# Performance work log

Measured on AMD Instinct MI355X. Metric: run time of the kernel, lower is better.

## Reference

```python
import math
import jax, jax.numpy as jnp
import numpy as np

B, S, HID = 2, 1024, 1024
NH, HD = 16, 64
WIN = 4096
CACHE = 3072
EPS = 1e-5


def _clinear(xr, xi, Wr, Wi, br, bi):
    # complex linear: (xr + i xi)(Wr + i Wi)^T + (br + i bi)
    yr = xr @ Wr.T - xi @ Wi.T + br
    yi = xr @ Wi.T + xi @ Wr.T + bi
    return yr, yi


def _forward(hidden_re, hidden_im, K_cache_re, K_cache_im, V_cache_re, V_cache_im,
             gamma, beta_re, beta_im,
             q_Wr, q_Wi, q_br, q_bi, k_Wr, k_Wi, k_br, k_bi,
             v_Wr, v_Wi, v_br, v_bi, o_Wr, o_Wi, o_br, o_bi):
    batch, seq, _ = hidden_re.shape
    # --- complex LayerNorm: center complex mean, normalize by sqrt(E|x-mu|^2) ---
    mur = hidden_re.mean(-1, keepdims=True)
    mui = hidden_im.mean(-1, keepdims=True)
    cr = hidden_re - mur
    ci = hidden_im - mui
    inv = jax.lax.rsqrt((cr * cr + ci * ci).mean(-1, keepdims=True) + EPS)
    nr = cr * inv * gamma + beta_re
    ni = ci * inv * gamma + beta_im
    # --- projections ---
    Qr, Qi = _clinear(nr, ni, q_Wr, q_Wi, q_br, q_bi)
    Kr, Ki = _clinear(nr, ni, k_Wr, k_Wi, k_br, k_bi)
    Vr, Vi = _clinear(nr, ni, v_Wr, v_Wi, v_br, v_bi)
    Qr = Qr.reshape(batch, seq, NH, HD)
    Qi = Qi.reshape(batch, seq, NH, HD)
    Kr = Kr.reshape(batch, seq, NH, HD)
    Ki = Ki.reshape(batch, seq, NH, HD)
    Vr = Vr.reshape(batch, seq, NH, HD)
    Vi = Vi.reshape(batch, seq, NH, HD)
    # --- KV cache concat + window eviction (static shapes) ---
    cache_len = K_cache_re.shape[1]
    Kr = jnp.concatenate([K_cache_re, Kr], axis=1)
    Ki = jnp.concatenate([K_cache_im, Ki], axis=1)
    Vr = jnp.concatenate([V_cache_re, Vr], axis=1)
    Vi = jnp.concatenate([V_cache_im, Vi], axis=1)
    total_kv = Kr.shape[1]
    if total_kv > WIN:
        drop = total_kv - WIN
        Kr, Ki, Vr, Vi = Kr[:, drop:], Ki[:, drop:], Vr[:, drop:], Vi[:, drop:]
        cache_len = max(0, cache_len - drop)
        total_kv = WIN
    # --- Hermitian scores: Re(Q K^H) = Qr.Kr + Qi.Ki ---
    scale = 1.0 / math.sqrt(HD)
    scores = (jnp.einsum('bshd,bthd->bhst', Qr, Kr)
              + jnp.einsum('bshd,bthd->bhst', Qi, Ki)) * scale
    rows = jnp.arange(seq)[:, None]
    cols = jnp.arange(total_kv)[None, :]
    allowed = cols <= rows + cache_len  # causal within current chunk, full cache visible
    scores = jnp.where(allowed, scores, jnp.float32(-1e30))
    weights = jax.nn.softmax(scores, axis=-1)  # [B,NH,S,T]
    outr = jnp.einsum('bhst,bthd->bshd', weights, Vr).reshape(batch, seq, NH * HD)
    outi = jnp.einsum('bhst,bthd->bshd', weights, Vi).reshape(batch, seq, NH * HD)
    dr, di = _clinear(outr, outi, o_Wr, o_Wi, o_br, o_bi)
    out_re = hidden_re + dr
    out_im = hidden_im + di
    new_K_re, new_K_im = Kr[:, -WIN:], Ki[:, -WIN:]
    new_V_re, new_V_im = Vr[:, -WIN:], Vi[:, -WIN:]
    return out_re, out_im, new_K_re, new_K_im, new_V_re, new_V_im


def setup_inputs() -> dict:
    key = jax.random.key(0)
    ks = jax.random.split(key, 16)
    w = 0.02
    d = {
        'hidden_re': jax.random.normal(ks[0], (B, S, HID), jnp.float32),
        'hidden_im': jax.random.normal(ks[1], (B, S, HID), jnp.float32),
        'K_cache_re': jax.random.normal(ks[2], (B, CACHE, NH, HD), jnp.float32),
        'K_cache_im': jax.random.normal(ks[3], (B, CACHE, NH, HD), jnp.float32),
        'V_cache_re': jax.random.normal(ks[4], (B, CACHE, NH, HD), jnp.float32),
        'V_cache_im': jax.random.normal(ks[5], (B, CACHE, NH, HD), jnp.float32),
        'gamma': jnp.ones((HID,), jnp.float32),
        'beta_re': jnp.zeros((HID,), jnp.float32),
        'beta_im': jnp.zeros((HID,), jnp.float32),
    }
    for i, p in enumerate(['q', 'k', 'v', 'o']):
        d[p + '_Wr'] = jax.random.normal(ks[6 + 2 * i], (HID, HID), jnp.float32) * w
        d[p + '_Wi'] = jax.random.normal(ks[7 + 2 * i], (HID, HID), jnp.float32) * w
        d[p + '_br'] = jnp.zeros((HID,), jnp.float32)
        d[p + '_bi'] = jnp.zeros((HID,), jnp.float32)
    return d


def reference(hidden_re, hidden_im, K_cache_re, K_cache_im, V_cache_re, V_cache_im,
              gamma, beta_re, beta_im,
              q_Wr, q_Wi, q_br, q_bi, k_Wr, k_Wi, k_br, k_bi,
              v_Wr, v_Wi, v_br, v_bi, o_Wr, o_Wi, o_br, o_bi):
    return _forward(hidden_re, hidden_im, K_cache_re, K_cache_im, V_cache_re, V_cache_im,
                    gamma, beta_re, beta_im,
                    q_Wr, q_Wi, q_br, q_bi, k_Wr, k_Wi, k_br, k_bi,
                    v_Wr, v_Wi, v_br, v_bi, o_Wr, o_Wi, o_br, o_bi)
```

## Files before the change

### kernel.cpp

```cpp
#include <hip/hip_runtime.h>
#include <hip/hip_bf16.h>
#include <cstdint>
#include <cstddef>

typedef __bf16 bf16x8 __attribute__((ext_vector_type(8)));
typedef float  f32x4  __attribute__((ext_vector_type(4)));

__device__ __forceinline__ unsigned short f2bf(float f) {
  union { float f; unsigned u; } v; v.f = f;
  unsigned u = v.u;
  u += 0x7FFFu + ((u >> 16) & 1u);
  return (unsigned short)(u >> 16);
}

__device__ __forceinline__ unsigned short f2bf_cvt(float f) {
  __bf16 h = (__bf16)f;
  return __builtin_bit_cast(unsigned short, h);
}

struct alignas(16) US8 { unsigned short u[8]; };

__device__ __forceinline__ void g2lds16(const void* g, void* l) {
  __builtin_amdgcn_global_load_lds(
      (const __attribute__((address_space(1))) unsigned int*)g,
      (__attribute__((address_space(3))) unsigned int*)l, 16, 0, 0);
}

#define BB 2
#define SS 1024
#define HID 1024
#define NHH 16
#define HDD 64
#define TT 4096
#define CCH 3072

__global__ __launch_bounds__(256) void ln_kernel(
    const float* __restrict__ hre, const float* __restrict__ him,
    const float* __restrict__ gamma, const float* __restrict__ bre,
    const float* __restrict__ bim, unsigned short* __restrict__ Aln)
{
  int m = blockIdx.x;
  int tid = threadIdx.x;
  const float4 vr = ((const float4*)(hre + (size_t)m * HID))[tid];
  const float4 vi = ((const float4*)(him + (size_t)m * HID))[tid];
  float sr = vr.x + vr.y + vr.z + vr.w;
  float si = vi.x + vi.y + vi.z + vi.w;
  float sq = vr.x*vr.x + vr.y*vr.y + vr.z*vr.z + vr.w*vr.w
           + vi.x*vi.x + vi.y*vi.y + vi.z*vi.z + vi.w*vi.w;
  __shared__ float red[3][4];
  int lane = tid & 63, w = tid >> 6;
  for (int off = 32; off; off >>= 1) {
    sr += __shfl_down(sr, off, 64);
    si += __shfl_down(si, off, 64);
    sq += __shfl_down(sq, off, 64);
  }
  if (lane == 0) { red[0][w] = sr; red[1][w] = si; red[2][w] = sq; }
  __syncthreads();
  sr = red[0][0] + red[0][1] + red[0][2] + red[0][3];
  si = red[1][0] + red[1][1] + red[1][2] + red[1][3];
  sq = red[2][0] + red[2][1] + red[2][2] + red[2][3];
  float mur = sr * (1.f/1024.f), mui = si * (1.f/1024.f);
  float var = sq * (1.f/1024.f) - mur*mur - mui*mui;
  float inv = rsqrtf(var + 1e-5f);
  int k = tid * 4;
  float4 g  = ((const float4*)gamma)[tid];
  float4 br = ((const float4*)bre)[tid];
  float4 bi = ((const float4*)bim)[tid];
  ushort4 nr, ni;
  nr.x = f2bf((vr.x - mur) * inv * g.x + br.x);
  nr.y = f2bf((vr.y - mur) * inv * g.y + br.y);
  nr.z = f2bf((vr.z - mur) * inv * g.z + br.z);
  nr.w = f2bf((vr.w - mur) * inv * g.w + br.w);
  ni.x = f2bf((vi.x - mui) * inv * g.x + bi.x);
  ni.y = f2bf((vi.y - mui) * inv * g.y + bi.y);
  ni.z = f2bf((vi.z - mui) * inv * g.z + bi.z);
  ni.w = f2bf((vi.w - mui) * inv * g.w + bi.w);
  *(ushort4*)&Aln[(size_t)m * 2048 + k]        = nr;
  *(ushort4*)&Aln[(size_t)m * 2048 + 1024 + k] = ni;
}

__global__ __launch_bounds__(256) void wprep_kernel(
    const float* __restrict__ qWr, const float* __restrict__ qWi,
    const float* __restrict__ kWr, const float* __restrict__ kWi,
    const float* __restrict__ vWr, const float* __restrict__ vWi,
    const float* __restrict__ oWr, const float* __restrict__ oWi,
    unsigned short* __restrict__ Wc)
{
  int gid = blockIdx.x * 256 + threadIdx.x;
  int idx = gid * 8;
  int p   = idx >> 22;
  int rem = idx & 0x3FFFFF;
  int n   = rem >> 11;
  int k   = rem & 2047;
  const float* Wr; const float* Wi;
  switch (p) {
    case 0:  Wr = qWr; Wi = qWi; break;
    case 1:  Wr = kWr; Wi = kWi; break;
    case 2:  Wr = vWr; Wi = vWi; break;
    default: Wr = oWr; Wi = oWi; break;
  }
  const float* src; float sgn = 1.f;
  if (n < 1024) {
    if (k < 1024) src = Wr + (size_t)n * 1024 + k;
    else        { src = Wi + (size_t)n * 1024 + (k - 1024); sgn = -1.f; }
  } else {
    if (k < 1024) src = Wi + (size_t)(n - 1024) * 1024 + k;
    else          src = Wr + (size_t)(n - 1024) * 1024 + (k - 1024);
  }
  float4 a = ((const float4*)src)[0];
  float4 b = ((const float4*)src)[1];
  US8 o;
  o.u[0] = f2bf(a.x * sgn); o.u[1] = f2bf(a.y * sgn);
  o.u[2] = f2bf(a.z * sgn); o.u[3] = f2bf(a.w * sgn);
  o.u[4] = f2bf(b.x * sgn); o.u[5] = f2bf(b.y * sgn);
  o.u[6] = f2bf(b.z * sgn); o.u[7] = f2bf(b.w * sgn);
  *(US8*)&Wc[idx] = o;
}

__global__ __launch_bounds__(256) void bprep_kernel(
    const float* __restrict__ qbr, const float* __restrict__ qbi,
    const float* __restrict__ kbr, const float* __restrict__ kbi,
    const float* __restrict__ vbr, const float* __restrict__ vbi,
    const float* __restrict__ obr, const float* __restrict__ obi,
    float* __restrict__ bc)
{
  int idx = blockIdx.x * 256 + threadIdx.x;
  int p = idx >> 11, n = idx & 2047;
  const float* br; const float* bi;
  switch (p) {
    case 0:  br = qbr; bi = qbi; break;
    case 1:  br = kbr; bi = kbi; break;
    case 2:  br = vbr; bi = vbi; break;
    default: br = obr; bi = obi; break;
  }
  bc[idx] = (n < 1024) ? br[n] : bi[n - 1024];
}

__global__ __launch_bounds__(256) void gemm_bt_kernel(
    const unsigned short* __restrict__ A, const unsigned short* __restrict__ Bm,
    const float* __restrict__ bias, float* __restrict__ C, int Nstride, int K)
{
  __shared__ alignas(16) unsigned short As[128][32];
  __shared__ alignas(16) unsigned short Bs[128][32];
  int bm = blockIdx.y * 128;
  int bn = blockIdx.x * 128;
  int tid = threadIdx.x;
  int lane = tid & 63, w = tid >> 6;
  int wm = (w >> 1) * 64, wn = (w & 1) * 64;
  int l15 = lane & 15, q = lane >> 4;
  int lr = tid >> 2;
  int lc = (tid & 3) * 8;

  f32x4 acc[4][4] = {};

  for (int k0 = 0; k0 < K; k0 += 32) {
    g2lds16(&A [(size_t)(bm + lr)      * K + k0 + lc], (unsigned short*)As + 8*tid);
    g2lds16(&A [(size_t)(bm + lr + 64) * K + k0 + lc], (unsigned short*)As + 2048 + 8*tid);
    g2lds16(&Bm[(size_t)(bn + lr)      * K + k0 + lc], (unsigned short*)Bs + 8*tid);
    g2lds16(&Bm[(size_t)(bn + lr + 64) * K + k0 + lc], (unsigned short*)Bs + 2048 + 8*tid);
    __syncthreads();
    bf16x8 af[4], bfr[4];
#pragma unroll
    for (int i = 0; i < 4; i++) af[i]  = *(const bf16x8*)&As[wm + i*16 + l15][q*8];
#pragma unroll
    for (int i = 0; i < 4; i++) bfr[i] = *(const bf16x8*)&Bs[wn + i*16 + l15][q*8];
#pragma unroll
    for (int i = 0; i < 4; i++)
#pragma unroll
      for (int j = 0; j < 4; j++)
        acc[i][j] = __builtin_amdgcn_mfma_f32_16x16x32_bf16(af[i], bfr[j], acc[i][j], 0, 0, 0);
    __syncthreads();
  }

#pragma unroll
  for (int i = 0; i < 4; i++)
#pragma unroll
    for (int j = 0; j < 4; j++) {
      int n = bn + wn + j*16 + l15;
      float bv = bias[n];
#pragma unroll
      for (int r = 0; r < 4; r++) {
        int m = bm + wm + i*16 + q*4 + r;
        C[(size_t)m * Nstride + n] = acc[i][j][r] + bv;
      }
    }
}

__global__ __launch_bounds__(256) void gemm_oproj_kernel(
    const unsigned short* __restrict__ A, const unsigned short* __restrict__ Bm,
    const float* __restrict__ bias, const float* __restrict__ hre,
    const float* __restrict__ him, float* __restrict__ out)
{
  __shared__ alignas(16) unsigned short As[128][32];
  __shared__ alignas(16) unsigned short Bs[128][32];
  int bm = blockIdx.y * 128;
  int bn = blockIdx.x * 128;
  int tid = threadIdx.x;
  int lane = tid & 63, w = tid >> 6;
  int wm = (w >> 1) * 64, wn = (w & 1) * 64;
  int l15 = lane & 15, q = lane >> 4;
  int lr = tid >> 2;
  int lc = (tid & 3) * 8;
  const int K = 2048;

  f32x4 acc[4][4] = {};

  for (int k0 = 0; k0 < K; k0 += 32) {
    g2lds16(&A [(size_t)(bm + lr)      * K + k0 + lc], (unsigned short*)As + 8*tid);
    g2lds16(&A [(size_t)(bm + lr + 64) * K + k0 + lc], (unsigned short*)As + 2048 + 8*tid);
    g2lds16(&Bm[(size_t)(bn + lr)      * K + k0 + lc], (unsigned short*)Bs + 8*tid);
    g2lds16(&Bm[(size_t)(bn + lr + 64) * K + k0 + lc], (unsigned short*)Bs + 2048 + 8*tid);
    __syncthreads();
    bf16x8 af[4], bfr[4];
#pragma unroll
    for (int i = 0; i < 4; i++) af[i]  = *(const bf16x8*)&As[wm + i*16 + l15][q*8];
#pragma unroll
    for (int i = 0; i < 4; i++) bfr[i] = *(const bf16x8*)&Bs[wn + i*16 + l15][q*8];
#pragma unroll
    for (int i = 0; i < 4; i++)
#pragma unroll
      for (int j = 0; j < 4; j++)
        acc[i][j] = __builtin_amdgcn_mfma_f32_16x16x32_bf16(af[i], bfr[j], acc[i][j], 0, 0, 0);
    __syncthreads();
  }

#pragma unroll
  for (int i = 0; i < 4; i++)
#pragma unroll
    for (int j = 0; j < 4; j++) {
      int n = bn + wn + j*16 + l15;
      float bv = bias[n];
#pragma unroll
      for (int r = 0; r < 4; r++) {
        int m = bm + wm + i*16 + q*4 + r;
        float val = acc[i][j][r] + bv;
        if (n < 1024) out[(size_t)m * 1024 + n] = val + hre[(size_t)m * 1024 + n];
        else out[2097152 + (size_t)m * 1024 + (n - 1024)] = val + him[(size_t)m * 1024 + (n - 1024)];
      }
    }
}

__global__ __launch_bounds__(256) void pack_q_kernel(
    const float* __restrict__ Cqkv, unsigned short* __restrict__ Qp)
{
  int gid = blockIdx.x * 256 + threadIdx.x;
  int idx = gid * 4;
  int d2 = idx & 127;
  int s  = (idx >> 7) & 1023;
  int bh = idx >> 17;
  int b = bh >> 4, h = bh & 15;
  int d = d2 & 63;
  int col = (d2 < 64) ? (h*64 + d) : (1024 + h*64 + d);
  float4 v = *(const float4*)&Cqkv[((size_t)b * 1024 + s) * 6144 + col];
  ushort4 o;
  o.x = f2bf(v.x * 0.125f); o.y = f2bf(v.y * 0.125f);
  o.z = f2bf(v.z * 0.125f); o.w = f2bf(v.w * 0.125f);
  *(ushort4*)&Qp[idx] = o;
}

__global__ __launch_bounds__(256) void pack_kv_kernel(
    const float* __restrict__ c_re, const float* __restrict__ c_im,
    const float* __restrict__ Cqkv, int colbase,
    unsigned short* __restrict__ Kp,
    float* __restrict__ out_re, float* __restrict__ out_im)
{
  int gid = blockIdx.x * 256 + threadIdx.x;
  int idx = gid * 4;
  int d2 = idx & 127;
  int t  = (idx >> 7) & 4095;
  int bh = idx >> 19;
  int b = bh >> 4, h = bh & 15;
  int d = d2 & 63;
  bool im = d2 >= 64;
  float4 v;
  if (t < CCH) {
    const float* src = im ? c_im : c_re;
    v = *(const float4*)&src[(((size_t)b * CCH + t) * 16 + h) * 64 + d];
  } else {
    int col = colbase + (im ? (1024 + h*64 + d) : (h*64 + d));
    v = *(const float4*)&Cqkv[((size_t)b * 1024 + (t - CCH)) * 6144 + col];
  }
  if (Kp) {
    ushort4 o;
    o.x = f2bf(v.x); o.y = f2bf(v.y); o.z = f2bf(v.z); o.w = f2bf(v.w);
    *(ushort4*)&Kp[idx] = o;
  }
  float* dst = im ? out_im : out_re;
  *(float4*)&dst[(((size_t)b * 4096 + t) * 16 + h) * 64 + d] = v;
}

__global__ __launch_bounds__(256) void pack_vt_kernel(
    const float* __restrict__ Vc_re, const float* __restrict__ Vc_im,
    const float* __restrict__ Cqkv, unsigned short* __restrict__ Vt)
{
  __shared__ float Ts[64][136];
  const int ty = blockIdx.x & 63;
  const int bh = blockIdx.x >> 6;
  const int b = bh >> 4, h = bh & 15;
  const int t0 = ty * 64;
  const int tid = threadIdx.x;
#pragma unroll
  for (int rr = 0; rr < 8; rr++) {
    int j = rr * 256 + tid;
    int t_loc = j >> 5, c = j & 31;
    int d2 = c * 4;
    int t = t0 + t_loc;
    float4 v;
    if (t < CCH) {
      const float* src = (d2 < 64) ? Vc_re : Vc_im;
      int d = (d2 < 64) ? d2 : d2 - 64;
      v = *(const float4*)&src[(((size_t)b * CCH + t) * 16 + h) * 64 + d];
    } else {
      int col = 4096 + ((d2 < 64) ? (h*64 + d2) : (1024 + h*64 + d2 - 64));
      v = *(const float4*)&Cqkv[((size_t)b * 1024 + (t - CCH)) * 6144 + col];
    }
    *(float4*)&Ts[t_loc][d2] = v;
  }
  __syncthreads();
  const int d2 = tid >> 1, half = tid & 1;
  unsigned short tmp[32];
#pragma unroll
  for (int i = 0; i < 32; i++) tmp[i] = f2bf(Ts[half*32 + i][d2]);
  size_t dst = (size_t)bh * 128 * 4096 + (size_t)d2 * 4096 + t0 + half*32;
#pragma unroll
  for (int kq = 0; kq < 4; kq++)
    *(US8*)&Vt[dst + kq*8] = *(US8*)&tmp[kq*8];
}

__global__ __launch_bounds__(256) void attn_kernel(
    const unsigned short* __restrict__ Qp, const unsigned short* __restrict__ Kp,
    const unsigned short* __restrict__ Vt, float* __restrict__ Opart,
    float* __restrict__ Lpart)
{
  const int bh   = blockIdx.x;
  const int sblk = blockIdx.y;
  const int tpar = blockIdx.z;
  const int s0 = sblk * 128;
  const int tid = threadIdx.x;
  const int lane = tid & 63, w = tid >> 6;
  const int l15 = lane & 15, q = lane >> 4;

  __shared__ alignas(16) unsigned short Ks[2][64][128];
  __shared__ alignas(16) unsigned short Vs[2][128][64];
  __shared__ alignas(16) unsigned short Ps[4][32][64];

  bf16x8 qf[2][4];
#pragma unroll
  for (int mi = 0; mi < 2; mi++) {
    const size_t qb = ((size_t)bh * 1024 + s0 + w*32 + mi*16 + l15) * 128;
#pragma unroll
    for (int kc = 0; kc < 4; kc++)
      qf[mi][kc] = *(const bf16x8*)&Qp[qb + kc*32 + q*8];
  }

  f32x4 oacc[2][8] = {};
  float lsum[2][4] = {};

  const size_t kpb = (size_t)bh * 4096 * 128;
  const size_t vtb = (size_t)bh * 128 * 4096;
  const int n_tiles = 2*sblk + 50;
  const int n_safe  = n_tiles - 2;

  auto issue = [&](int buf, int t0) {
#pragma unroll
    for (int kk = 0; kk < 4; kk++) {
      int j = (w*4 + kk)*64 + lane;
      int r = j >> 4, p = j & 15, c = p ^ (r & 7);
      g2lds16(&Kp[kpb + (size_t)(t0 + r) * 128 + c*8],
              (unsigned short*)&Ks[buf][0][0] + (size_t)j * 8);
    }
#pragma unroll
    for (int kk = 0; kk < 4; kk++) {
      int j = (w*4 + kk)*64 + lane;
      int r = j >> 3, p = j & 7, c = p ^ (r & 7);
      g2lds16(&Vt[vtb + (size_t)r * 4096 + t0 + c*8],
              (unsigned short*)&Vs[buf][0][0] + (size_t)j * 8);
    }
  };

  int buf = 0;
  issue(0, tpar * 64);

  for (int it = tpar; it < n_tiles; it += 2) {
    __syncthreads();
    if (it + 2 < n_tiles) issue(buf ^ 1, (it + 2) * 64);

    f32x4 sacc[2][4] = {};
#pragma unroll
    for (int kc = 0; kc < 4; kc++) {
      bf16x8 kf[4];
#pragma unroll
      for (int nc = 0; nc < 4; nc++)
        kf[nc] = *(const bf16x8*)&Ks[buf][nc*16 + l15][((kc*4 + q) ^ (l15 & 7)) * 8];
#pragma unroll
      for (int mi = 0; mi < 2; mi++)
#pragma unroll
        for (int nc = 0; nc < 4; nc++)
          sacc[mi][nc] = __builtin_amdgcn_mfma_f32_16x16x32_bf16(qf[mi][kc], kf[nc], sacc[mi][nc], 0, 0, 0);
    }

    const bool safe = (it < n_safe);
    const int t0 = it << 6;
#pragma unroll
    for (int mi = 0; mi < 2; mi++)
#pragma unroll
      for (int r = 0; r < 4; r++) {
        const int rr = mi*16 + q*4 + r;
        const int rel = s0 + w*32 + rr + CCH - t0;
        float ls = 0.f;
#pragma unroll
        for (int nc = 0; nc < 4; nc++) {
          float p = __expf(sacc[mi][nc][r]);
          if (!safe && (nc*16 + l15 > rel)) p = 0.f;
          ls += p;
          int cch = ((nc*2 + (l15 >> 3)) ^ (rr & 7));
          Ps[w][rr][cch*8 + (l15 & 7)] = f2bf_cvt(p);
        }
        lsum[mi][r] += ls;
      }

#pragma unroll
    for (int kch = 0; kch < 2; kch++) {
      bf16x8 pf[2];
#pragma unroll
      for (int mi = 0; mi < 2; mi++) {
        int rr = mi*16 + l15;
        pf[mi] = *(const bf16x8*)&Ps[w][rr][((kch*4 + q) ^ (rr & 7)) * 8];
      }
#pragma unroll
      for (int dc = 0; dc < 8; dc++) {
        int d2 = dc*16 + l15;
        bf16x8 vfr = *(const bf16x8*)&Vs[buf][d2][((kch*4 + q) ^ (l15 & 7)) * 8];
#pragma unroll
        for (int mi = 0; mi < 2; mi++)
          oacc[mi][dc] = __builtin_amdgcn_mfma_f32_16x16x32_bf16(pf[mi], vfr, oacc[mi][dc], 0, 0, 0);
      }
    }
    buf ^= 1;
  }

  const size_t pb = ((size_t)tpar * 32 + bh) * 1024 + s0 + w*32;
#pragma unroll
  for (int mi = 0; mi < 2; mi++)
#pragma unroll
    for (int r = 0; r < 4; r++) {
      float l = lsum[mi][r];
      l += __shfl_xor(l, 1, 64);
      l += __shfl_xor(l, 2, 64);
      l += __shfl_xor(l, 4, 64);
      l += __shfl_xor(l, 8, 64);
      if (l15 == 0) Lpart[pb + mi*16 + q*4 + r] = l;
    }
#pragma unroll
  for (int mi = 0; mi < 2; mi++)
#pragma unroll
    for (int dc = 0; dc < 8; dc++)
#pragma unroll
      for (int r = 0; r < 4; r++)
        Opart[(pb + mi*16 + q*4 + r) * 128 + dc*16 + l15] = oacc[mi][dc][r];
}

__global__ __launch_bounds__(256) void attn_combine_kernel(
    const float* __restrict__ Opart, const float* __restrict__ Lpart,
    unsigned short* __restrict__ Ao)
{
  const size_t TS = 4194304ull;
  int gid = blockIdx.x * 256 + threadIdx.x;
  int idx = gid * 8;
  int m = idx >> 11, n0 = idx & 2047;
  int b = m >> 10, s = m & 1023;
  int h, d2_0;
  if (n0 < 1024) { h = n0 >> 6; d2_0 = n0 & 63; }
  else { h = (n0 - 1024) >> 6; d2_0 = 64 + ((n0 - 1024) & 63); }
  int bh = b*16 + h;
  size_t ob = ((size_t)bh * 1024 + s) * 128 + d2_0;
  float l0 = Lpart[(size_t)bh * 1024 + s];
  float l1 = Lpart[TS/128 + (size_t)bh * 1024 + s];
  float inv = 1.f / (l0 + l1);
  float4 x0 = *(const float4*)&Opart[ob];
  float4 x1 = *(const float4*)&Opart[ob + 4];
  float4 y0 = *(const float4*)&Opart[ob + TS];
  float4 y1 = *(const float4*)&Opart[ob + TS + 4];
  US8 o;
  o.u[0] = f2bf((x0.x + y0.x) * inv); o.u[1] = f2bf((x0.y + y0.y) * inv);
  o.u[2] = f2bf((x0.z + y0.z) * inv); o.u[3] = f2bf((x0.w + y0.w) * inv);
  o.u[4] = f2bf((x1.x + y1.x) * inv); o.u[5] = f2bf((x1.y + y1.y) * inv);
  o.u[6] = f2bf((x1.z + y1.z) * inv); o.u[7] = f2bf((x1.w + y1.w) * inv);
  *(US8*)&Ao[idx] = o;
}

extern "C" void kernel_launch(void* const* d_in, const int* in_sizes, int n_in,
                              void* d_out, int out_size, void* d_ws, size_t ws_size,
                              hipStream_t stream)
{
  (void)in_sizes; (void)n_in; (void)out_size; (void)ws_size;
  const float* hre = (const float*)d_in[0];
  const float* him = (const float*)d_in[1];
  const float* Kcr = (const float*)d_in[2];
  const float* Kci = (const float*)d_in[3];
  const float* Vcr = (const float*)d_in[4];
  const float* Vci = (const float*)d_in[5];
  const float* gamma = (const float*)d_in[6];
  const float* bre = (const float*)d_in[7];
  const float* bim = (const float*)d_in[8];
  const float* qWr = (const float*)d_in[9];
  const float* qWi = (const float*)d_in[10];
  const float* qbr = (const float*)d_in[11];
  const float* qbi = (const float*)d_in[12];
  const float* kWr = (const float*)d_in[13];
  const float* kWi = (const float*)d_in[14];
  const float* kbr = (const float*)d_in[15];
  const float* kbi = (const float*)d_in[16];
  const float* vWr = (const float*)d_in[17];
  const float* vWi = (const float*)d_in[18];
  const float* vbr = (const float*)d_in[19];
  const float* vbi = (const float*)d_in[20];
  const float* oWr = (const float*)d_in[21];
  const float* oWi = (const float*)d_in[22];
  const float* obr = (const float*)d_in[23];
  const float* obi = (const float*)d_in[24];
  float* out = (float*)d_out;

  char* ws = (char*)d_ws;
  size_t off = 0;
  auto carve = [&](size_t bytes) {
    char* p = ws + off;
    off += (bytes + 255) & ~(size_t)255;
    return p;
  };
  unsigned short* Aln = (unsigned short*)carve(2048ull * 2048 * 2);
  unsigned short* Wc  = (unsigned short*)carve(4ull * 2048 * 2048 * 2);
  float*          bc  = (float*)carve(4ull * 2048 * 4);
  float*          Cqkv= (float*)carve(2048ull * 6144 * 4);
  unsigned short* Qp  = (unsigned short*)carve(4194304ull * 2);
  unsigned short* Kp  = (unsigned short*)carve(16777216ull * 2);
  unsigned short* Vt  = (unsigned short*)carve(16777216ull * 2);
  unsigned short* Ao  = (unsigned short*)carve(2048ull * 2048 * 2);

  float* Opart = (float*)Cqkv;
  float* Lpart = (float*)Aln;

  float* out_Kre = out + 4194304;
  float* out_Kim = out + 4194304 + 8388608;
  float* out_Vre = out + 4194304 + 2 * 8388608;
  float* out_Vim = out + 4194304 + 3 * 8388608;

  hipLaunchKernelGGL(ln_kernel, dim3(2048), dim3(256), 0, stream,
                     hre, him, gamma, bre, bim, Aln);
  hipLaunchKernelGGL(wprep_kernel, dim3(8192), dim3(256), 0, stream,
                     qWr, qWi, kWr, kWi, vWr, vWi, oWr, oWi, Wc);
  hipLaunchKernelGGL(bprep_kernel, dim3(32), dim3(256), 0, stream,
                     qbr, qbi, kbr, kbi, vbr, vbi, obr, obi, bc);
  hipLaunchKernelGGL(gemm_bt_kernel, dim3(48, 16), dim3(256), 0, stream,
                     Aln, Wc, bc, Cqkv, 6144, 2048);
  hipLaunchKernelGGL(pack_q_kernel, dim3(4096), dim3(256), 0, stream, Cqkv, Qp);
  hipLaunchKernelGGL(pack_kv_kernel, dim3(16384), dim3(256), 0, stream,
                     Kcr, Kci, Cqkv, 2048, Kp, out_Kre, out_Kim);
  hipLaunchKernelGGL(pack_kv_kernel, dim3(16384), dim3(256), 0, stream,
                     Vcr, Vci, Cqkv, 4096, (unsigned short*)nullptr, out_Vre, out_Vim);
  hipLaunchKernelGGL(pack_vt_kernel, dim3(2048), dim3(256), 0, stream,
                     Vcr, Vci, Cqkv, Vt);
  hipLaunchKernelGGL(attn_kernel, dim3(32, 8, 2), dim3(256), 0, stream,
                     Qp, Kp, Vt, Opart, Lpart);
  hipLaunchKernelGGL(attn_combine_kernel, dim3(2048), dim3(256), 0, stream,
                     Opart, Lpart, Ao);
  hipLaunchKernelGGL(gemm_oproj_kernel, dim3(16, 16), dim3(256), 0, stream,
                     Ao, Wc + 3ull * 2048 * 2048, bc + 3 * 2048, hre, him, out);
}
```

Baseline: 609.9 us.

## Fuse QKV packing into GEMM epilogue and tune attention exp, priority and swizzle

```diff
diff --git a/kernel.cpp b/kernel.cpp
--- a/kernel.cpp
+++ b/kernel.cpp
@@ -33,6 +33,7 @@
 #define HDD 64
 #define TT 4096
 #define CCH 3072
+#define QSCALE (0.125f * 1.44269504088896f)
 
 __global__ __launch_bounds__(256) void ln_kernel(
     const float* __restrict__ hre, const float* __restrict__ him,
@@ -136,12 +137,16 @@
   bc[idx] = (n < 1024) ? br[n] : bi[n - 1024];
 }
 
-__global__ __launch_bounds__(256) void gemm_bt_kernel(
+__global__ __launch_bounds__(256) void gemm_qkv_kernel(
     const unsigned short* __restrict__ A, const unsigned short* __restrict__ Bm,
-    const float* __restrict__ bias, float* __restrict__ C, int Nstride, int K)
+    const float* __restrict__ bias,
+    unsigned short* __restrict__ Qp, unsigned short* __restrict__ Kp,
+    float* __restrict__ out_Kre, float* __restrict__ out_Kim,
+    float* __restrict__ out_Vre, float* __restrict__ out_Vim)
 {
   __shared__ alignas(16) unsigned short As[128][32];
   __shared__ alignas(16) unsigned short Bs[128][32];
+  const int K = 2048;
   int bm = blockIdx.y * 128;
   int bn = blockIdx.x * 128;
   int tid = threadIdx.x;
@@ -172,16 +177,35 @@
     __syncthreads();
   }
 
+  const int sec = bn >> 11;
 #pragma unroll
   for (int i = 0; i < 4; i++)
 #pragma unroll
     for (int j = 0; j < 4; j++) {
       int n = bn + wn + j*16 + l15;
       float bv = bias[n];
+      int col = n & 2047;
+      int re = (col < 1024) ? 1 : 0;
+      int h = (col & 1023) >> 6, d = col & 63;
+      int d2 = re ? d : 64 + d;
 #pragma unroll
       for (int r = 0; r < 4; r++) {
         int m = bm + wm + i*16 + q*4 + r;
-        C[(size_t)m * Nstride + n] = acc[i][j][r] + bv;
+        float val = acc[i][j][r] + bv;
+        int b = m >> 10, s = m & 1023;
+        int bh = b*16 + h;
+        if (sec == 0) {
+          Qp[((size_t)bh*1024 + s)*128 + d2] = f2bf(val * QSCALE);
+        } else if (sec == 1) {
+          int t = CCH + s;
+          Kp[((size_t)bh*4096 + t)*128 + d2] = f2bf(val);
+          float* dst = re ? out_Kre : out_Kim;
+          dst[(((size_t)b*4096 + t)*16 + h)*64 + d] = val;
+        } else {
+          int t = CCH + s;
+          float* dst = re ? out_Vre : out_Vim;
+          dst[(((size_t)b*4096 + t)*16 + h)*64 + d] = val;
+        }
       }
     }
 }
@@ -240,58 +264,31 @@
     }
 }
 
-__global__ __launch_bounds__(256) void pack_q_kernel(
-    const float* __restrict__ Cqkv, unsigned short* __restrict__ Qp)
-{
-  int gid = blockIdx.x * 256 + threadIdx.x;
-  int idx = gid * 4;
-  int d2 = idx & 127;
-  int s  = (idx >> 7) & 1023;
-  int bh = idx >> 17;
-  int b = bh >> 4, h = bh & 15;
-  int d = d2 & 63;
-  int col = (d2 < 64) ? (h*64 + d) : (1024 + h*64 + d);
-  float4 v = *(const float4*)&Cqkv[((size_t)b * 1024 + s) * 6144 + col];
-  ushort4 o;
-  o.x = f2bf(v.x * 0.125f); o.y = f2bf(v.y * 0.125f);
-  o.z = f2bf(v.z * 0.125f); o.w = f2bf(v.w * 0.125f);
-  *(ushort4*)&Qp[idx] = o;
-}
-
-__global__ __launch_bounds__(256) void pack_kv_kernel(
+__global__ __launch_bounds__(256) void pack_kcache_kernel(
     const float* __restrict__ c_re, const float* __restrict__ c_im,
-    const float* __restrict__ Cqkv, int colbase,
     unsigned short* __restrict__ Kp,
     float* __restrict__ out_re, float* __restrict__ out_im)
 {
-  int gid = blockIdx.x * 256 + threadIdx.x;
-  int idx = gid * 4;
+  int bh = blockIdx.y;
+  int idx = (blockIdx.x * 256 + threadIdx.x) * 4;
   int d2 = idx & 127;
-  int t  = (idx >> 7) & 4095;
-  int bh = idx >> 19;
+  int t  = idx >> 7;
   int b = bh >> 4, h = bh & 15;
   int d = d2 & 63;
   bool im = d2 >= 64;
-  float4 v;
-  if (t < CCH) {
-    const float* src = im ? c_im : c_re;
-    v = *(const float4*)&src[(((size_t)b * CCH + t) * 16 + h) * 64 + d];
-  } else {
-    int col = colbase + (im ? (1024 + h*64 + d) : (h*64 + d));
-    v = *(const float4*)&Cqkv[((size_t)b * 1024 + (t - CCH)) * 6144 + col];
-  }
-  if (Kp) {
-    ushort4 o;
-    o.x = f2bf(v.x); o.y = f2bf(v.y); o.z = f2bf(v.z); o.w = f2bf(v.w);
-    *(ushort4*)&Kp[idx] = o;
-  }
+  const float* src = im ? c_im : c_re;
+  float4 v = *(const float4*)&src[(((size_t)b * CCH + t) * 16 + h) * 64 + d];
+  ushort4 o;
+  o.x = f2bf(v.x); o.y = f2bf(v.y); o.z = f2bf(v.z); o.w = f2bf(v.w);
+  *(ushort4*)&Kp[((size_t)bh * 4096 + t) * 128 + d2] = o;
   float* dst = im ? out_im : out_re;
   *(float4*)&dst[(((size_t)b * 4096 + t) * 16 + h) * 64 + d] = v;
 }
 
-__global__ __launch_bounds__(256) void pack_vt_kernel(
+__global__ __launch_bounds__(256) void pack_vt_fused_kernel(
     const float* __restrict__ Vc_re, const float* __restrict__ Vc_im,
-    const float* __restrict__ Cqkv, unsigned short* __restrict__ Vt)
+    float* __restrict__ out_Vre, float* __restrict__ out_Vim,
+    unsigned short* __restrict__ Vt)
 {
   __shared__ float Ts[64][136];
   const int ty = blockIdx.x & 63;
@@ -305,14 +302,16 @@
     int t_loc = j >> 5, c = j & 31;
     int d2 = c * 4;
     int t = t0 + t_loc;
+    int d = (d2 < 64) ? d2 : d2 - 64;
     float4 v;
     if (t < CCH) {
       const float* src = (d2 < 64) ? Vc_re : Vc_im;
-      int d = (d2 < 64) ? d2 : d2 - 64;
       v = *(const float4*)&src[(((size_t)b * CCH + t) * 16 + h) * 64 + d];
+      float* dst = (d2 < 64) ? out_Vre : out_Vim;
+      *(float4*)&dst[(((size_t)b * 4096 + t) * 16 + h) * 64 + d] = v;
     } else {
-      int col = 4096 + ((d2 < 64) ? (h*64 + d2) : (1024 + h*64 + d2 - 64));
-      v = *(const float4*)&Cqkv[((size_t)b * 1024 + (t - CCH)) * 6144 + col];
+      const float* src = (d2 < 64) ? out_Vre : out_Vim;
+      v = *(const float4*)&src[(((size_t)b * 4096 + t) * 16 + h) * 64 + d];
     }
     *(float4*)&Ts[t_loc][d2] = v;
   }
@@ -386,6 +385,7 @@
     if (it + 2 < n_tiles) issue(buf ^ 1, (it + 2) * 64);
 
     f32x4 sacc[2][4] = {};
+    __builtin_amdgcn_s_setprio(1);
 #pragma unroll
     for (int kc = 0; kc < 4; kc++) {
       bf16x8 kf[4];
@@ -398,6 +398,7 @@
         for (int nc = 0; nc < 4; nc++)
           sacc[mi][nc] = __builtin_amdgcn_mfma_f32_16x16x32_bf16(qf[mi][kc], kf[nc], sacc[mi][nc], 0, 0, 0);
     }
+    __builtin_amdgcn_s_setprio(0);
 
     const bool safe = (it < n_safe);
     const int t0 = it << 6;
@@ -410,10 +411,11 @@
         float ls = 0.f;
 #pragma unroll
         for (int nc = 0; nc < 4; nc++) {
-          float p = __expf(sacc[mi][nc][r]);
+          float p;
+          asm("v_exp_f32 %0, %1" : "=v"(p) : "v"(sacc[mi][nc][r]));
           if (!safe && (nc*16 + l15 > rel)) p = 0.f;
           ls += p;
-          int cch = ((nc*2 + (l15 >> 3)) ^ (rr & 7));
+          int cch = (nc*2 + (l15 >> 3)) ^ ((q << 1) | (r & 1));
           Ps[w][rr][cch*8 + (l15 & 7)] = f2bf_cvt(p);
         }
         lsum[mi][r] += ls;
@@ -425,8 +427,10 @@
 #pragma unroll
       for (int mi = 0; mi < 2; mi++) {
         int rr = mi*16 + l15;
-        pf[mi] = *(const bf16x8*)&Ps[w][rr][((kch*4 + q) ^ (rr & 7)) * 8];
+        int sw = (((l15 >> 2) & 3) << 1) | (l15 & 1);
+        pf[mi] = *(const bf16x8*)&Ps[w][rr][((kch*4 + q) ^ sw) * 8];
       }
+      __builtin_amdgcn_s_setprio(1);
 #pragma unroll
       for (int dc = 0; dc < 8; dc++) {
         int d2 = dc*16 + l15;
@@ -435,6 +439,7 @@
         for (int mi = 0; mi < 2; mi++)
           oacc[mi][dc] = __builtin_amdgcn_mfma_f32_16x16x32_bf16(pf[mi], vfr, oacc[mi][dc], 0, 0, 0);
       }
+      __builtin_amdgcn_s_setprio(0);
     }
     buf ^= 1;
   }
@@ -475,7 +480,7 @@
   int bh = b*16 + h;
   size_t ob = ((size_t)bh * 1024 + s) * 128 + d2_0;
   float l0 = Lpart[(size_t)bh * 1024 + s];
-  float l1 = Lpart[TS/128 + (size_t)bh * 1024 + s];
+  float l1 = Lpart[32768 + (size_t)bh * 1024 + s];
   float inv = 1.f / (l0 + l1);
   float4 x0 = *(const float4*)&Opart[ob];
   float4 x1 = *(const float4*)&Opart[ob + 4];
@@ -528,17 +533,15 @@
     off += (bytes + 255) & ~(size_t)255;
     return p;
   };
-  unsigned short* Aln = (unsigned short*)carve(2048ull * 2048 * 2);
-  unsigned short* Wc  = (unsigned short*)carve(4ull * 2048 * 2048 * 2);
-  float*          bc  = (float*)carve(4ull * 2048 * 4);
-  float*          Cqkv= (float*)carve(2048ull * 6144 * 4);
-  unsigned short* Qp  = (unsigned short*)carve(4194304ull * 2);
-  unsigned short* Kp  = (unsigned short*)carve(16777216ull * 2);
-  unsigned short* Vt  = (unsigned short*)carve(16777216ull * 2);
-  unsigned short* Ao  = (unsigned short*)carve(2048ull * 2048 * 2);
-
-  float* Opart = (float*)Cqkv;
-  float* Lpart = (float*)Aln;
+  unsigned short* Aln  = (unsigned short*)carve(2048ull * 2048 * 2);
+  unsigned short* Wc   = (unsigned short*)carve(4ull * 2048 * 2048 * 2);
+  float*          bc   = (float*)carve(4ull * 2048 * 4);
+  unsigned short* Qp   = (unsigned short*)carve(4194304ull * 2);
+  unsigned short* Kp   = (unsigned short*)carve(16777216ull * 2);
+  unsigned short* Vt   = (unsigned short*)carve(16777216ull * 2);
+  unsigned short* Ao   = (unsigned short*)carve(2048ull * 2048 * 2);
+  float*          Opart= (float*)carve(2ull * 32 * 1024 * 128 * 4);
+  float*          Lpart= (float*)carve(2ull * 32 * 1024 * 4);
 
   float* out_Kre = out + 4194304;
   float* out_Kim = out + 4194304 + 8388608;
@@ -551,15 +554,12 @@
                      qWr, qWi, kWr, kWi, vWr, vWi, oWr, oWi, Wc);
   hipLaunchKernelGGL(bprep_kernel, dim3(32), dim3(256), 0, stream,
                      qbr, qbi, kbr, kbi, vbr, vbi, obr, obi, bc);
-  hipLaunchKernelGGL(gemm_bt_kernel, dim3(48, 16), dim3(256), 0, stream,
-                     Aln, Wc, bc, Cqkv, 6144, 2048);
-  hipLaunchKernelGGL(pack_q_kernel, dim3(4096), dim3(256), 0, stream, Cqkv, Qp);
-  hipLaunchKernelGGL(pack_kv_kernel, dim3(16384), dim3(256), 0, stream,
-                     Kcr, Kci, Cqkv, 2048, Kp, out_Kre, out_Kim);
-  hipLaunchKernelGGL(pack_kv_kernel, dim3(16384), dim3(256), 0, stream,
-                     Vcr, Vci, Cqkv, 4096, (unsigned short*)nullptr, out_Vre, out_Vim);
-  hipLaunchKernelGGL(pack_vt_kernel, dim3(2048), dim3(256), 0, stream,
-                     Vcr, Vci, Cqkv, Vt);
+  hipLaunchKernelGGL(gemm_qkv_kernel, dim3(48, 16), dim3(256), 0, stream,
+                     Aln, Wc, bc, Qp, Kp, out_Kre, out_Kim, out_Vre, out_Vim);
+  hipLaunchKernelGGL(pack_kcache_kernel, dim3(384, 32), dim3(256), 0, stream,
+                     Kcr, Kci, Kp, out_Kre, out_Kim);
+  hipLaunchKernelGGL(pack_vt_fused_kernel, dim3(2048), dim3(256), 0, stream,
+                     Vcr, Vci, out_Vre, out_Vim, Vt);
   hipLaunchKernelGGL(attn_kernel, dim3(32, 8, 2), dim3(256), 0, stream,
                      Qp, Kp, Vt, Opart, Lpart);
   hipLaunchKernelGGL(attn_combine_kernel, dim3(2048), dim3(256), 0, stream,
```

Result: no change. 601.6 us (-1.4%).
